# Kernel optimization log

Hardware: AMD Instinct MI355X
Metric: run time of the kernel (lower is better)

The kernel has to match this reference:

```python
import jax, jax.numpy as jnp
import numpy as np

B, T, S = 256, 32, 128
I, H, O = 256, 1024, 256


def setup_inputs() -> dict:
    key = jax.random.key(0)
    ks = jax.random.split(key, 8)
    sc = 0.02
    return {
        "shifted_target": jax.random.normal(ks[0], (B, T, I), jnp.float32),
        "encoder_outputs": jax.random.normal(ks[1], (B, S, H), jnp.float32),
        "W_ih": jax.random.normal(ks[2], (4 * H, I), jnp.float32) * sc,
        "W_hh": jax.random.normal(ks[3], (4 * H, H), jnp.float32) * sc,
        "b_ih": jax.random.normal(ks[4], (4 * H,), jnp.float32) * sc,
        "b_hh": jax.random.normal(ks[5], (4 * H,), jnp.float32) * sc,
        "W_fc": jax.random.normal(ks[6], (O, 2 * H), jnp.float32) * sc,
        "b_fc": jax.random.normal(ks[7], (O,), jnp.float32) * sc,
    }


def reference(shifted_target, encoder_outputs, W_ih, W_hh, b_ih, b_hh, W_fc, b_fc):
    bs, tgt_len, inp = shifted_target.shape
    hid = encoder_outputs.shape[-1]
    # torch code feeds zeros (not shifted_target[:,0]) at t=0, with zero init state
    xs = shifted_target.at[:, 0, :].set(0.0)
    xs = jnp.swapaxes(xs, 0, 1)  # [T, B, I]

    def step(carry, x_t):
        h, c = carry
        gates = x_t @ W_ih.T + b_ih + h @ W_hh.T + b_hh  # [B, 4H]
        i, f, g, o = jnp.split(gates, 4, axis=-1)
        i = jax.nn.sigmoid(i)
        f = jax.nn.sigmoid(f)
        g = jnp.tanh(g)
        o = jax.nn.sigmoid(o)
        c = f * c + i * g
        h = o * jnp.tanh(c)
        # dot-product attention against encoder states
        score = jnp.einsum('bh,bsh->bs', h, encoder_outputs)
        prob = jax.nn.softmax(score, axis=-1)
        ctx = jnp.einsum('bs,bsh->bh', prob, encoder_outputs)
        out_t = jnp.concatenate([ctx, h], axis=-1) @ W_fc.T + b_fc
        return (h, c), (out_t, prob)

    h0 = jnp.zeros((bs, hid), shifted_target.dtype)
    c0 = jnp.zeros((bs, hid), shifted_target.dtype)
    _, (outs, probs) = jax.lax.scan(step, (h0, c0), xs)
    return jnp.swapaxes(outs, 0, 1), jnp.swapaxes(probs, 0, 1)
```

## Files before the change

### kernel.cpp

```cpp
#include <hip/hip_runtime.h>
#include <math.h>

#define B_  256
#define T_  32
#define S_  128
#define I_  256
#define H_  1024
#define O_  256
#define G4  4096
#define K2  2048

typedef __attribute__((ext_vector_type(8))) short bf16x8;
typedef __attribute__((ext_vector_type(4))) float f32x4;

#define MFMA16(a, b, c) __builtin_amdgcn_mfma_f32_16x16x32_bf16(a, b, c, 0, 0, 0)

__device__ __forceinline__ unsigned short f2bf(float f) {
    unsigned int u = __float_as_uint(f);
    u = (u + 0x7FFFu + ((u >> 16) & 1u)) >> 16;
    return (unsigned short)u;
}
__device__ __forceinline__ float sigm(float x) { return 1.0f / (1.0f + __expf(-x)); }

__device__ __forceinline__ bf16x8 ldg_sys(const unsigned short* p) {
    bf16x8 r;
    asm volatile("global_load_dwordx4 %0, %1, off sc0 sc1"
                 : "=v"(r) : "v"(p) : "memory");
    return r;
}
__device__ __forceinline__ void stg_sys16(unsigned short* p, unsigned short v) {
    asm volatile("global_store_short %0, %1, off sc0 sc1"
                 :: "v"(p), "v"(v) : "memory");
}

__global__ void prep_kernel(
    const float* __restrict__ x, const float* __restrict__ enc,
    const float* __restrict__ Wih, const float* __restrict__ Whh,
    const float* __restrict__ bih, const float* __restrict__ bhh,
    const float* __restrict__ Wfc,
    unsigned short* __restrict__ WihR, unsigned short* __restrict__ WhhR,
    unsigned short* __restrict__ WfcR, float* __restrict__ biasR,
    unsigned short* __restrict__ xs, unsigned short* __restrict__ encB,
    unsigned short* __restrict__ h0, unsigned short* __restrict__ h1,
    unsigned* __restrict__ bar)
{
    if (blockIdx.x == 0 && threadIdx.x == 0) { bar[0] = 0u; bar[1] = 0u; }

    const long NWHH = (long)G4 * H_;
    const long NWIH = (long)G4 * I_;
    const long NWFC = (long)O_ * K2;
    const long NB   = G4;
    const long NX   = (long)B_ * T_ * I_;
    const long NE   = (long)B_ * S_ * H_;
    const long NH   = (long)B_ * H_;
    const long total = NWHH + NWIH + NWFC + NB + NX + NE + 2 * NH;
    for (long i = (long)blockIdx.x * blockDim.x + threadIdx.x; i < total;
         i += (long)gridDim.x * blockDim.x) {
        long j = i;
        if (j < NE) { encB[j] = f2bf(enc[j]); continue; }
        j -= NE;
        if (j < NWHH) {
            int r = (int)(j >> 10), k = (int)(j & 1023);
            int n = ((r & 1023) << 2) | (r >> 10);
            WhhR[(long)n * H_ + k] = f2bf(Whh[j]);
            continue;
        }
        j -= NWHH;
        if (j < NWIH) {
            int r = (int)(j >> 8), k = (int)(j & 255);
            int n = ((r & 1023) << 2) | (r >> 10);
            WihR[(long)n * I_ + k] = f2bf(Wih[j]);
            continue;
        }
        j -= NWIH;
        if (j < NWFC) { WfcR[j] = f2bf(Wfc[j]); continue; }
        j -= NWFC;
        if (j < NB) {
            int r = (int)j;
            int n = ((r & 1023) << 2) | (r >> 10);
            biasR[n] = bih[r] + bhh[r];
            continue;
        }
        j -= NB;
        if (j < NX) {
            int t = (int)((j >> 8) & 31);
            xs[j] = (t == 0) ? (unsigned short)0 : f2bf(x[j]);
            continue;
        }
        j -= NX;
        if (j < NH) { h0[j] = 0; continue; }
        j -= NH;
        h1[j] = 0;
    }
}

__global__ __launch_bounds__(512, 2) void steps_kernel(
    const unsigned short* __restrict__ xs,
    const unsigned short* __restrict__ WihR,
    const unsigned short* __restrict__ WhhR,
    const float* __restrict__ biasR,
    unsigned short* __restrict__ h0b,
    unsigned short* __restrict__ h1b,
    unsigned short* __restrict__ hall,
    unsigned* __restrict__ bar)
{
    __shared__ unsigned short Wlds[64 * 1024];
    __shared__ float Gs[64 * 68];

    const int tid = threadIdx.x;
    const int lane = tid & 63, wave = tid >> 6;
    const int quad = lane >> 4, l16 = lane & 15;
    const int wm = wave >> 2, wn = wave & 3;

    const int id = blockIdx.x;
    const int xcd = id & 7, slot = id >> 3;
    const int n0 = (xcd * 8 + (slot >> 2)) * 64;
    const int m0 = (slot & 3) * 64;

    for (int i = 0; i < 16; i++) {
        int q = i * 512 + tid;
        int row = q >> 7, kc = q & 127;
        int e = kc * 8;
        int de = row * 1024 + (e ^ ((row & 7) << 3));
        *(uint4*)(Wlds + de) = *(const uint4*)(WhhR + (long)(n0 + row) * H_ + e);
    }

    const int nw = n0 + wn * 16 + l16;
    bf16x8 bwx[8];
    {
        const unsigned short* px = WihR + (long)nw * I_ + quad * 8;
#pragma unroll
        for (int kk = 0; kk < 8; kk++) bwx[kk] = *(const bf16x8*)(px + kk * 32);
    }
    const float bj = biasR[nw];

    const unsigned short* bbase = Wlds + (wn * 16 + l16) * 1024;
    const int swz = (l16 & 7) << 3;

    const unsigned short* xrow[2];
    long hoff[2];
#pragma unroll
    for (int i = 0; i < 2; i++) {
        int ar = m0 + wm * 32 + i * 16 + l16;
        xrow[i] = xs + (long)ar * T_ * I_ + quad * 8;
        hoff[i] = (long)ar * H_ + quad * 8;
    }

    float c_reg[2] = {0.f, 0.f};

    unsigned target = 0;

    __syncthreads();

#pragma unroll 1
    for (int t = 0; t < T_; t++) {
        const unsigned short* hp = (t & 1) ? h1b : h0b;
        unsigned short* hn = (t & 1) ? h0b : h1b;

        const f32x4 z = {0.f, 0.f, 0.f, 0.f};
        f32x4 acc[2] = {z, z};

        {
            bf16x8 a[8][2];
#pragma unroll
            for (int kk = 0; kk < 8; kk++)
#pragma unroll
                for (int i = 0; i < 2; i++)
                    a[kk][i] = *(const bf16x8*)(xrow[i] + (long)t * I_ + kk * 32);
#pragma unroll
            for (int kk = 0; kk < 8; kk++)
#pragma unroll
                for (int i = 0; i < 2; i++)
                    acc[i] = MFMA16(a[kk][i], bwx[kk], acc[i]);
        }

        if (t > 0) {
            if (tid == 0) {
                int spins = 0;
                while (__hip_atomic_load(bar, __ATOMIC_RELAXED,
                                         __HIP_MEMORY_SCOPE_AGENT) < target &&
                       spins < (1 << 20)) {
                    __builtin_amdgcn_s_sleep(2);
                    ++spins;
                }
            }
            __syncthreads();
            __builtin_amdgcn_sched_barrier(0);
        }

#pragma unroll
        for (int kc = 0; kc < 4; kc++) {
            bf16x8 a[8][2];
#pragma unroll
            for (int kk = 0; kk < 8; kk++)
#pragma unroll
                for (int i = 0; i < 2; i++)
                    a[kk][i] = ldg_sys(hp + hoff[i] + (long)(kc * 8 + kk) * 32);
            bf16x8 bb[8];
#pragma unroll
            for (int kk = 0; kk < 8; kk++) {
                int e = ((kc * 8 + kk) * 32 + quad * 8) ^ swz;
                bb[kk] = *(const bf16x8*)(bbase + e);
            }
            asm volatile("s_waitcnt vmcnt(0)" ::: "memory");
            __builtin_amdgcn_sched_barrier(0);
#pragma unroll
            for (int kk = 0; kk < 8; kk++)
#pragma unroll
                for (int i = 0; i < 2; i++)
                    acc[i] = MFMA16(a[kk][i], bb[kk], acc[i]);
        }

#pragma unroll
        for (int i = 0; i < 2; i++)
#pragma unroll
            for (int r = 0; r < 4; r++)
                Gs[(wm * 32 + i * 16 + quad * 4 + r) * 68 + wn * 16 + l16] =
                    acc[i][r] + bj;
        __syncthreads();

#pragma unroll
        for (int j = 0; j < 2; j++) {
            int p = j * 512 + tid;
            int row = p >> 4, u = p & 15;
            float gi = Gs[row * 68 + u * 4 + 0];
            float gf = Gs[row * 68 + u * 4 + 1];
            float gg = Gs[row * 68 + u * 4 + 2];
            float go = Gs[row * 68 + u * 4 + 3];
            int b = m0 + row;
            int jg = (n0 >> 2) + u;
            float ii = sigm(gi), ff = sigm(gf), g3 = tanhf(gg), oo = sigm(go);
            float cn = ff * c_reg[j] + ii * g3;
            float hh = oo * tanhf(cn);
            c_reg[j] = cn;
            unsigned short hb = f2bf(hh);
            stg_sys16(hn + (long)b * H_ + jg, hb);
            hall[((long)b * T_ + t) * H_ + jg] = hb;
        }

        if (t < T_ - 1) {
            asm volatile("s_waitcnt vmcnt(0)" ::: "memory");
            __syncthreads();
            if (tid == 0)
                __hip_atomic_fetch_add(bar, 1u, __ATOMIC_RELAXED,
                                       __HIP_MEMORY_SCOPE_AGENT);
            target += 256;
        }
    }
}

__global__ __launch_bounds__(256) void scores_kernel(
    const unsigned short* __restrict__ hall,
    const unsigned short* __restrict__ encB,
    float* __restrict__ probs,
    unsigned short* __restrict__ PB)
{
    __shared__ float Sc[32 * 132];

    const int tid = threadIdx.x;
    const int lane = tid & 63, wave = tid >> 6;
    const int quad = lane >> 4, l16 = lane & 15;
    const int b = blockIdx.x;
    const int nw = wave;

    const unsigned short* pa0 = hall + ((long)b * T_ + l16) * H_ + quad * 8;
    const unsigned short* pa1 = hall + ((long)b * T_ + 16 + l16) * H_ + quad * 8;
    const unsigned short* pb0 = encB + ((long)b * S_ + nw * 32 + l16) * H_ + quad * 8;
    const unsigned short* pb1 = pb0 + 16 * H_;

    const f32x4 z = {0.f, 0.f, 0.f, 0.f};
    f32x4 acc00 = z, acc01 = z, acc10 = z, acc11 = z;

#pragma unroll 4
    for (int k0 = 0; k0 < H_; k0 += 32) {
        bf16x8 a0 = *(const bf16x8*)(pa0 + k0);
        bf16x8 a1 = *(const bf16x8*)(pa1 + k0);
        bf16x8 b0 = *(const bf16x8*)(pb0 + k0);
        bf16x8 b1 = *(const bf16x8*)(pb1 + k0);
        acc00 = MFMA16(a0, b0, acc00);
        acc01 = MFMA16(a0, b1, acc01);
        acc10 = MFMA16(a1, b0, acc10);
        acc11 = MFMA16(a1, b1, acc11);
    }
#pragma unroll
    for (int r = 0; r < 4; r++) {
        int row0 = quad * 4 + r;
        int col0 = nw * 32 + l16;
        Sc[row0 * 132 + col0]            = acc00[r];
        Sc[row0 * 132 + col0 + 16]       = acc01[r];
        Sc[(row0 + 16) * 132 + col0]      = acc10[r];
        Sc[(row0 + 16) * 132 + col0 + 16] = acc11[r];
    }
    __syncthreads();
    for (int r = 0; r < 8; r++) {
        int row = wave * 8 + r;
        float v0 = Sc[row * 132 + lane];
        float v1 = Sc[row * 132 + 64 + lane];
        float mx = fmaxf(v0, v1);
#pragma unroll
        for (int off = 32; off > 0; off >>= 1) mx = fmaxf(mx, __shfl_xor(mx, off));
        float e0 = __expf(v0 - mx), e1 = __expf(v1 - mx);
        float s = e0 + e1;
#pragma unroll
        for (int off = 32; off > 0; off >>= 1) s += __shfl_xor(s, off);
        float inv = 1.0f / s;
        float p0 = e0 * inv, p1 = e1 * inv;
        long o = ((long)b * T_ + row) * S_;
        probs[o + lane] = p0;
        probs[o + 64 + lane] = p1;
        PB[o + lane] = f2bf(p0);
        PB[o + 64 + lane] = f2bf(p1);
    }
}

__global__ __launch_bounds__(256) void ctx_kernel(
    const unsigned short* __restrict__ encB,
    const unsigned short* __restrict__ PB,
    unsigned short* __restrict__ ctxo)
{
    __shared__ unsigned short Es[S_ * 256];

    const int tid = threadIdx.x;
    const int lane = tid & 63, wave = tid >> 6;
    const int quad = lane >> 4, l16 = lane & 15;
    const int b = blockIdx.x;
    const int h0 = blockIdx.y * 256;

    for (int i = tid; i < S_ * 32; i += 256) {
        int s = i >> 5, hc = (i & 31) * 8;
        *(uint4*)(Es + s * 256 + hc) =
            *(const uint4*)(encB + ((long)b * S_ + s) * H_ + h0 + hc);
    }
    bf16x8 a[2][4];
#pragma unroll
    for (int i = 0; i < 2; i++)
#pragma unroll
        for (int ks = 0; ks < 4; ks++)
            a[i][ks] = *(const bf16x8*)(PB + ((long)b * T_ + i * 16 + l16) * S_ +
                                        ks * 32 + quad * 8);
    __syncthreads();

    f32x4 acc[2][4];
    const f32x4 z = {0.f, 0.f, 0.f, 0.f};
#pragma unroll
    for (int i = 0; i < 2; i++)
#pragma unroll
        for (int j = 0; j < 4; j++) acc[i][j] = z;

    const int cw = wave * 64;
#pragma unroll
    for (int ks = 0; ks < 4; ks++) {
        const int kb = ks * 32 + quad * 8;
#pragma unroll
        for (int j = 0; j < 4; j++) {
            const int col = cw + j * 16 + l16;
            bf16x8 bb;
#pragma unroll
            for (int e = 0; e < 8; e++) bb[e] = (short)Es[(kb + e) * 256 + col];
            acc[0][j] = MFMA16(a[0][ks], bb, acc[0][j]);
            acc[1][j] = MFMA16(a[1][ks], bb, acc[1][j]);
        }
    }
#pragma unroll
    for (int i = 0; i < 2; i++)
#pragma unroll
        for (int j = 0; j < 4; j++)
#pragma unroll
            for (int r = 0; r < 4; r++) {
                int row = i * 16 + quad * 4 + r;
                int col = h0 + cw + j * 16 + l16;
                ctxo[((long)b * T_ + row) * H_ + col] = f2bf(acc[i][j][r]);
            }
}

__global__ __launch_bounds__(256) void fc_kernel(
    const unsigned short* __restrict__ ctxo,
    const unsigned short* __restrict__ hall,
    const unsigned short* __restrict__ WfcR,
    const float* __restrict__ bfc,
    float* __restrict__ out)
{
    __shared__ __align__(16) unsigned short As[64 * 40];
    __shared__ __align__(16) unsigned short Bs[128 * 40];

    const int tid = threadIdx.x;
    const int lane = tid & 63, wave = tid >> 6;
    const int wm = wave >> 1, wn = wave & 1;
    const int quad = lane >> 4, l16 = lane & 15;
    const int n0 = blockIdx.x * 128, m0 = blockIdx.y * 64;

    const int arow = tid >> 2, akc = (tid & 3) * 8;
    const int brow = tid >> 1, bkc = (tid & 1) * 16;

    f32x4 acc[2][4];
    const f32x4 z = {0.f, 0.f, 0.f, 0.f};
#pragma unroll
    for (int i = 0; i < 2; i++)
#pragma unroll
        for (int j = 0; j < 4; j++) acc[i][j] = z;

    for (int k0 = 0; k0 < K2; k0 += 32) {
        const unsigned short* asrc = (k0 < H_)
            ? ctxo + (long)(m0 + arow) * H_ + k0 + akc
            : hall + (long)(m0 + arow) * H_ + (k0 - H_) + akc;
        *(uint4*)(As + arow * 40 + akc) = *(const uint4*)asrc;
        const unsigned short* src = WfcR + (long)(n0 + brow) * K2 + k0 + bkc;
        *(uint4*)(Bs + brow * 40 + bkc)     = *(const uint4*)src;
        *(uint4*)(Bs + brow * 40 + bkc + 8) = *(const uint4*)(src + 8);
        __syncthreads();
        bf16x8 a0 = *(const bf16x8*)(As + (wm * 32 + l16) * 40 + quad * 8);
        bf16x8 a1 = *(const bf16x8*)(As + (wm * 32 + 16 + l16) * 40 + quad * 8);
#pragma unroll
        for (int j = 0; j < 4; j++) {
            bf16x8 bb = *(const bf16x8*)(Bs + (wn * 64 + j * 16 + l16) * 40 + quad * 8);
            acc[0][j] = MFMA16(a0, bb, acc[0][j]);
            acc[1][j] = MFMA16(a1, bb, acc[1][j]);
        }
        __syncthreads();
    }
#pragma unroll
    for (int i = 0; i < 2; i++)
#pragma unroll
        for (int j = 0; j < 4; j++)
#pragma unroll
            for (int r = 0; r < 4; r++) {
                int row = m0 + wm * 32 + i * 16 + quad * 4 + r;
                int col = n0 + wn * 64 + j * 16 + l16;
                out[(long)row * O_ + col] = acc[i][j][r] + bfc[col];
            }
}

extern "C" void kernel_launch(void* const* d_in, const int* in_sizes, int n_in,
                              void* d_out, int out_size, void* d_ws, size_t ws_size,
                              hipStream_t stream) {
    const float* x   = (const float*)d_in[0];
    const float* enc = (const float*)d_in[1];
    const float* Wih = (const float*)d_in[2];
    const float* Whh = (const float*)d_in[3];
    const float* bih = (const float*)d_in[4];
    const float* bhh = (const float*)d_in[5];
    const float* Wfc = (const float*)d_in[6];
    const float* bfc = (const float*)d_in[7];
    float* out = (float*)d_out;

    char* ws = (char*)d_ws;
    unsigned short* WIHR = (unsigned short*)(ws + 0);
    unsigned short* WHHR = (unsigned short*)(ws + 2097152);
    unsigned short* WFCR = (unsigned short*)(ws + 10485760);
    float*          BIAS = (float*)         (ws + 11534336);
    unsigned short* XS   = (unsigned short*)(ws + 11550720);
    unsigned short* H0   = (unsigned short*)(ws + 15745024);
    unsigned short* H1   = (unsigned short*)(ws + 16269312);
    unsigned*       BAR  = (unsigned*)      (ws + 16793600);
    unsigned short* HALL = (unsigned short*)(ws + 17842176);
    unsigned short* ENCB = (unsigned short*)(ws + 34619392);
    unsigned short* PB   = (unsigned short*)(ws + 101728256);
    unsigned short* CTX  = (unsigned short*)(ws + 103825408);

    prep_kernel<<<8192, 256, 0, stream>>>(x, enc, Wih, Whh, bih, bhh, Wfc,
                                          WIHR, WHHR, WFCR, BIAS, XS, ENCB,
                                          H0, H1, BAR);

    {
        void* args[] = {(void*)&XS, (void*)&WIHR, (void*)&WHHR, (void*)&BIAS,
                        (void*)&H0, (void*)&H1, (void*)&HALL, (void*)&BAR};
        hipLaunchCooperativeKernel(reinterpret_cast<void*>(steps_kernel),
                                   dim3(256), dim3(512), args, 0, stream);
    }

    scores_kernel<<<B_, 256, 0, stream>>>(HALL, ENCB,
                                          out + (long)B_ * T_ * O_, PB);
    ctx_kernel<<<dim3(B_, 4), 256, 0, stream>>>(ENCB, PB, CTX);
    fc_kernel<<<dim3(2, 128), 256, 0, stream>>>(CTX, HALL, WFCR, bfc, out);
}
```

Before: 0.9996 ms.

## Replace global atomic-counter barrier with per-row-tile flag arrays

Replaces the single global atomic counter that all 256 blocks incremented each timestep with per-block flags. Each block now waits only on the 64 blocks sharing its batch tile (same m0), since those produce the h rows it reads. One wave polls the 64 flags in parallel with system-coherent loads, and the sleep interval is shortened. This removes atomic contention and decouples independent batch tiles, at the cost of more polling traffic.

Measured after the change: 1.010 ms. Within noise of the previous version (+1.0%).

```diff
diff --git a/kernel.cpp b/kernel.cpp
--- a/kernel.cpp
+++ b/kernel.cpp
@@ -30,6 +30,16 @@
 }
 __device__ __forceinline__ void stg_sys16(unsigned short* p, unsigned short v) {
     asm volatile("global_store_short %0, %1, off sc0 sc1"
+                 :: "v"(p), "v"(v) : "memory");
+}
+__device__ __forceinline__ unsigned ldg_flag(const unsigned* p) {
+    unsigned r;
+    asm volatile("global_load_dword %0, %1, off sc0 sc1\n\ts_waitcnt vmcnt(0)"
+                 : "=v"(r) : "v"(p) : "memory");
+    return r;
+}
+__device__ __forceinline__ void stg_flag(unsigned* p, unsigned v) {
+    asm volatile("global_store_dword %0, %1, off sc0 sc1"
                  :: "v"(p), "v"(v) : "memory");
 }
 
@@ -44,7 +54,7 @@
     unsigned short* __restrict__ h0, unsigned short* __restrict__ h1,
     unsigned* __restrict__ bar)
 {
-    if (blockIdx.x == 0 && threadIdx.x == 0) { bar[0] = 0u; bar[1] = 0u; }
+    if (blockIdx.x == 0 && threadIdx.x < 256) bar[threadIdx.x] = 0u;
 
     const long NWHH = (long)G4 * H_;
     const long NWIH = (long)G4 * I_;
@@ -114,8 +124,12 @@
 
     const int id = blockIdx.x;
     const int xcd = id & 7, slot = id >> 3;
-    const int n0 = (xcd * 8 + (slot >> 2)) * 64;
-    const int m0 = (slot & 3) * 64;
+    const int nt = slot >> 2, mt = slot & 3;
+    const int n0 = (xcd * 8 + nt) * 64;
+    const int m0 = mt * 64;
+
+    unsigned* myflag = bar + mt * 64 + xcd * 8 + nt;
+    const unsigned* gflags = bar + mt * 64;
 
     for (int i = 0; i < 16; i++) {
         int q = i * 512 + tid;
@@ -148,8 +162,6 @@
 
     float c_reg[2] = {0.f, 0.f};
 
-    unsigned target = 0;
-
     __syncthreads();
 
 #pragma unroll 1
@@ -175,12 +187,11 @@
         }
 
         if (t > 0) {
-            if (tid == 0) {
+            if (tid < 64) {
                 int spins = 0;
-                while (__hip_atomic_load(bar, __ATOMIC_RELAXED,
-                                         __HIP_MEMORY_SCOPE_AGENT) < target &&
+                while (ldg_flag(gflags + tid) < (unsigned)t &&
                        spins < (1 << 20)) {
-                    __builtin_amdgcn_s_sleep(2);
+                    __builtin_amdgcn_s_sleep(1);
                     ++spins;
                 }
             }
@@ -241,10 +252,7 @@
         if (t < T_ - 1) {
             asm volatile("s_waitcnt vmcnt(0)" ::: "memory");
             __syncthreads();
-            if (tid == 0)
-                __hip_atomic_fetch_add(bar, 1u, __ATOMIC_RELAXED,
-                                       __HIP_MEMORY_SCOPE_AGENT);
-            target += 256;
+            if (tid == 0) stg_flag(myflag, (unsigned)(t + 1));
         }
     }
 }
```
